# Kernel tuning notes

Hardware: AMD Instinct MI355X
Metric: run time of the kernel (lower is better)

## Reference

```python
import jax, jax.numpy as jnp
import numpy as np

B, T, C = 4, 2048, 1024   # batch, seq_len, n_embd
H, D = 16, 64             # num heads, head dim (H*D == C)


def setup_inputs() -> dict:
    key = jax.random.key(0)
    ks = jax.random.split(key, 6)
    scale = 0.02
    x = jax.random.normal(ks[0], (B, T, C), dtype=jnp.float32)
    Wq = jax.random.normal(ks[1], (H, C, D), dtype=jnp.float32) * scale
    Wk = jax.random.normal(ks[2], (H, C, D), dtype=jnp.float32) * scale
    Wv = jax.random.normal(ks[3], (H, C, D), dtype=jnp.float32) * scale
    Wp = jax.random.normal(ks[4], (C, C), dtype=jnp.float32) * scale
    bp = jnp.zeros((C,), dtype=jnp.float32)
    return {"x": x, "Wq": Wq, "Wk": Wk, "Wv": Wv, "Wp": Wp, "bp": bp}


def reference(x, Wq, Wk, Wv, Wp, bp):
    # Batched per-head projections (equivalent to the per-head nn.Linear loop)
    q = jnp.einsum('btc,hcd->bhtd', x, Wq)
    k = jnp.einsum('btc,hcd->bhtd', x, Wk)
    v = jnp.einsum('btc,hcd->bhtd', x, Wv)
    # NOTE: original code scales by C**-0.5 where C = n_embd (not head dim)
    scores = jnp.einsum('bhtd,bhsd->bhts', q, k) * (C ** -0.5)
    causal = jnp.tril(jnp.ones((T, T), dtype=bool))  # [T, T]
    scores = jnp.where(causal, scores, -jnp.inf)
    att = jax.nn.softmax(scores, axis=-1)            # [B, H, T, T]
    out = jnp.einsum('bhts,bhsd->bhtd', att, v)      # [B, H, T, D]
    # concat heads (order matches torch.cat over head list) then output proj
    out = out.transpose(0, 2, 1, 3).reshape(B, T, H * D)
    return out @ Wp + bp
```

## Files before the change

### kernel.cpp

```cpp
#include <hip/hip_runtime.h>
#include <hip/hip_bf16.h>


#define B_ 4
#define T_ 2048
#define C_ 1024
#define H_ 16
#define D_ 64
#define M_ (B_*T_)

typedef unsigned short u16;
typedef unsigned short ushort8 __attribute__((ext_vector_type(8)));
typedef unsigned int uint4v __attribute__((ext_vector_type(4)));
typedef int int2v __attribute__((ext_vector_type(2)));
typedef __attribute__((ext_vector_type(8))) short bf16x8;
typedef __attribute__((ext_vector_type(16))) float f32x16;

__device__ __forceinline__ u16 f2bf(float f) {
    __hip_bfloat16 h = __float2bfloat16(f);
    return *reinterpret_cast<u16*>(&h);
}
__device__ __forceinline__ unsigned pkt(float lo, float hi2) {
    return __builtin_amdgcn_perm(__float_as_uint(hi2), __float_as_uint(lo), 0x07060302u);
}
__device__ __forceinline__ void gload_lds16(const void* g, void* lds) {
    __builtin_amdgcn_global_load_lds((const __attribute__((address_space(1))) unsigned int*)g,
                                     (__attribute__((address_space(3))) unsigned int*)lds, 16, 0, 0);
}
__device__ __forceinline__ int swz4(int r) { return (r ^ (r >> 2)) & 3; }

__global__ __launch_bounds__(256) void cast_x(const float* __restrict__ in, u16* __restrict__ out) {
    int i = (blockIdx.x * 256 + threadIdx.x) * 8;
    float4 a = *reinterpret_cast<const float4*>(in + i);
    float4 b = *reinterpret_cast<const float4*>(in + i + 4);
    ushort8 o;
    o[0]=f2bf(a.x); o[1]=f2bf(a.y); o[2]=f2bf(a.z); o[3]=f2bf(a.w);
    o[4]=f2bf(b.x); o[5]=f2bf(b.y); o[6]=f2bf(b.z); o[7]=f2bf(b.w);
    *reinterpret_cast<ushort8*>(out + i) = o;
}

__device__ __forceinline__ void ttile64(const float* __restrict__ in, int ldin,
                                        u16* __restrict__ out, int ldout, float scale) {
    __shared__ float t[64][65];
    const int tid = threadIdx.x;
    {
        int c = tid & 63, rr = tid >> 6;
        #pragma unroll
        for (int i = 0; i < 16; ++i) {
            int r = i * 4 + rr;
            t[r][c] = in[(size_t)r * ldin + c];
        }
    }
    __syncthreads();
    {
        int r2 = tid & 63, cg = tid >> 6;
        #pragma unroll
        for (int i = 0; i < 16; ++i) {
            int cc = i * 4 + cg;
            out[(size_t)cc * ldout + r2] = f2bf(t[r2][cc] * scale);
        }
    }
}

__global__ __launch_bounds__(256) void tw_qkv(const float* __restrict__ Wq, const float* __restrict__ Wk,
                                              const float* __restrict__ Wv, u16* __restrict__ Wt) {
    const int z = blockIdx.y;
    const int which = z >> 4, h = z & 15;
    const float* W = (which == 0 ? Wq : which == 1 ? Wk : Wv) + (size_t)h * C_ * D_;
    const int r0 = blockIdx.x * 64;
    const float scale = (which == 0) ? 0.03125f * 1.4426950408889634f : 1.f;
    ttile64(W + (size_t)r0 * D_, D_, Wt + (size_t)(which * 16 + h) * 64 * C_ + r0, C_, scale);
}

__global__ __launch_bounds__(256) void tw_p(const float* __restrict__ Wp, u16* __restrict__ Wpt) {
    const int r0 = blockIdx.x * 64, c0 = blockIdx.y * 64;
    ttile64(Wp + (size_t)r0 * C_ + c0, C_, Wpt + (size_t)c0 * C_ + r0, C_, 1.f);
}

__global__ __launch_bounds__(256) void tv(const u16* __restrict__ v, u16* __restrict__ vT) {
    __shared__ u16 t[64][72];
    const int tid = threadIdx.x;
    const int t0 = blockIdx.x * 64, bh = blockIdx.y;
    const u16* src = v + ((size_t)bh * T_ + t0) * D_;
    #pragma unroll
    for (int it = 0; it < 2; ++it) {
        int idx = it * 256 + tid;
        int r = idx >> 3, c8 = (idx & 7) * 8;
        *reinterpret_cast<ushort8*>(&t[r][c8]) =
            *reinterpret_cast<const ushort8*>(src + (size_t)r * D_ + c8);
    }
    __syncthreads();
    #pragma unroll
    for (int it = 0; it < 2; ++it) {
        int idx = it * 256 + tid;
        int d = idx >> 3, c8 = (idx & 7) * 8;
        ushort8 w;
        #pragma unroll
        for (int i = 0; i < 8; ++i) w[i] = t[c8 + i][d];
        *reinterpret_cast<ushort8*>(vT + ((size_t)bh * D_ + d) * T_ + t0 + c8) = w;
    }
}

__device__ __forceinline__ void gemm_core3(const u16* __restrict__ A, const u16* __restrict__ Bt,
                                           int m0, int n0, u16* lds, f32x16 (&acc)[4][2]) {
    const int tid = threadIdx.x;
    const int wid = tid >> 6, lane = tid & 63;
    const int l31 = lane & 31, hi = lane >> 5;
    const int wr = wid >> 1, wc = wid & 1;

    const u16* src[6];
    #pragma unroll
    for (int it = 0; it < 6; ++it) {
        int slot = it * 256 + tid;
        int row, g;
        const u16* base;
        if (it < 4) { row = slot >> 2; g = slot & 3; base = A + (size_t)(m0 + row) * C_; }
        else        { int s2 = slot - 1024; row = s2 >> 2; g = s2 & 3; base = Bt + (size_t)(n0 + row) * C_; }
        src[it] = base + ((g ^ swz4(row)) * 8);
    }

    const char* lb = reinterpret_cast<const char*>(lds);
    int aoff[2][4], boff[2][2];
    #pragma unroll
    for (int kk = 0; kk < 2; ++kk) {
        #pragma unroll
        for (int mt = 0; mt < 4; ++mt) {
            int row = wr * 128 + mt * 32 + l31;
            aoff[kk][mt] = row * 64 + (((kk * 2 + hi) ^ swz4(row)) & 3) * 16;
        }
        #pragma unroll
        for (int nt = 0; nt < 2; ++nt) {
            int row = wc * 64 + nt * 32 + l31;
            boff[kk][nt] = 16384 + row * 64 + (((kk * 2 + hi) ^ swz4(row)) & 3) * 16;
        }
    }

#define STG(BU16)                                                                   \
    {                                                                               \
        _Pragma("unroll")                                                           \
        for (int it = 0; it < 6; ++it) {                                            \
            gload_lds16(src[it], lds + (BU16) + (it * 256 + tid) * 8);              \
            src[it] += 32;                                                          \
        }                                                                           \
    }

    STG(0);
    STG(12288);

    #pragma unroll
    for (int t = 0; t < 32; ++t) {
        if (t < 31) { asm volatile("s_waitcnt vmcnt(6)" ::: "memory"); }
        else        { asm volatile("s_waitcnt vmcnt(0)" ::: "memory"); }
        __builtin_amdgcn_sched_barrier(0);
        __builtin_amdgcn_s_barrier();
        __builtin_amdgcn_sched_barrier(0);

        const char* lbuf = lb + (t & 1) * 24576;
        __builtin_amdgcn_s_setprio(1);
        #pragma unroll
        for (int kk = 0; kk < 2; ++kk) {
            bf16x8 bf0 = *reinterpret_cast<const bf16x8*>(lbuf + boff[kk][0]);
            bf16x8 bf1 = *reinterpret_cast<const bf16x8*>(lbuf + boff[kk][1]);
            #pragma unroll
            for (int mt = 0; mt < 4; ++mt) {
                bf16x8 af = *reinterpret_cast<const bf16x8*>(lbuf + aoff[kk][mt]);
                acc[mt][0] = __builtin_amdgcn_mfma_f32_32x32x16_bf16(af, bf0, acc[mt][0], 0, 0, 0);
                acc[mt][1] = __builtin_amdgcn_mfma_f32_32x32x16_bf16(af, bf1, acc[mt][1], 0, 0, 0);
            }
        }
        __builtin_amdgcn_s_setprio(0);
        __builtin_amdgcn_sched_barrier(0);
        __builtin_amdgcn_s_barrier();
        __builtin_amdgcn_sched_barrier(0);
        if (t + 2 < 32) STG((t & 1) * 12288);
    }
#undef STG
}

__global__ __launch_bounds__(256, 2) void qkv_gemm(const u16* __restrict__ xb, const u16* __restrict__ Wt,
                                                   u16* __restrict__ q, u16* __restrict__ k,
                                                   u16* __restrict__ v) {
    __shared__ u16 lds[2 * 12288];
    f32x16 acc[4][2];
    #pragma unroll
    for (int i = 0; i < 4; ++i)
        #pragma unroll
        for (int j = 0; j < 2; ++j)
            #pragma unroll
            for (int r = 0; r < 16; ++r) acc[i][j][r] = 0.f;
    const int m0 = blockIdx.x * 256, n0 = blockIdx.y * 128;
    gemm_core3(xb, Wt, m0, n0, lds, acc);

    const int tid = threadIdx.x, wid = tid >> 6, lane = tid & 63;
    const int l31 = lane & 31, hi = lane >> 5;
    const int wr = wid >> 1, wc = wid & 1;
    #pragma unroll
    for (int mt = 0; mt < 4; ++mt) {
        #pragma unroll
        for (int nt = 0; nt < 2; ++nt) {
            int n = n0 + wc * 64 + nt * 32 + l31;
            int which = n >> 10, h = (n >> 6) & 15, d = n & 63;
            u16* dst = (which == 0 ? q : which == 1 ? k : v);
            #pragma unroll
            for (int r = 0; r < 16; ++r) {
                int m = m0 + wr * 128 + mt * 32 + (r & 3) + 8 * (r >> 2) + 4 * hi;
                int b = m >> 11, t = m & (T_ - 1);
                dst[((size_t)(b * H_ + h) * T_ + t) * D_ + d] = f2bf(acc[mt][nt][r]);
            }
        }
    }
}

__global__ __launch_bounds__(256, 2) void out_gemm(const u16* __restrict__ ob, const u16* __restrict__ Wpt,
                                                   const float* __restrict__ bp, float* __restrict__ out) {
    __shared__ u16 lds[2 * 12288];
    f32x16 acc[4][2];
    #pragma unroll
    for (int i = 0; i < 4; ++i)
        #pragma unroll
        for (int j = 0; j < 2; ++j)
            #pragma unroll
            for (int r = 0; r < 16; ++r) acc[i][j][r] = 0.f;
    const int m0 = blockIdx.x * 256, n0 = blockIdx.y * 128;
    gemm_core3(ob, Wpt, m0, n0, lds, acc);

    const int tid = threadIdx.x, wid = tid >> 6, lane = tid & 63;
    const int l31 = lane & 31, hi = lane >> 5;
    const int wr = wid >> 1, wc = wid & 1;
    #pragma unroll
    for (int mt = 0; mt < 4; ++mt) {
        #pragma unroll
        for (int nt = 0; nt < 2; ++nt) {
            int n = n0 + wc * 64 + nt * 32 + l31;
            float bv = bp[n];
            #pragma unroll
            for (int r = 0; r < 16; ++r) {
                int m = m0 + wr * 128 + mt * 32 + (r & 3) + 8 * (r >> 2) + 4 * hi;
                out[(size_t)m * C_ + n] = acc[mt][nt][r] + bv;
            }
        }
    }
}

template<int CUR>
__device__ __forceinline__ void attn_tile(const char* const (&pf)[4], const bf16x8 (&qf)[4],
                                          const f32x16& z16, float& lrun,
                                          f32x16& oacc0, f32x16& oacc1,
                                          bool isdiag, int relq, int hi) {
    f32x16 st0, st1;
    __builtin_amdgcn_s_setprio(1);
    {
        bf16x8 ka0 = *reinterpret_cast<const bf16x8*>(pf[0] + CUR * 32768);
        bf16x8 ka1 = *reinterpret_cast<const bf16x8*>(pf[0] + CUR * 32768 + 4096);
        st0 = __builtin_amdgcn_mfma_f32_32x32x16_bf16(ka0, qf[0], z16, 0, 0, 0);
        st1 = __builtin_amdgcn_mfma_f32_32x32x16_bf16(ka1, qf[0], z16, 0, 0, 0);
    }
    #pragma unroll
    for (int kc = 1; kc < 4; ++kc) {
        bf16x8 ka0 = *reinterpret_cast<const bf16x8*>(pf[kc] + CUR * 32768);
        bf16x8 ka1 = *reinterpret_cast<const bf16x8*>(pf[kc] + CUR * 32768 + 4096);
        st0 = __builtin_amdgcn_mfma_f32_32x32x16_bf16(ka0, qf[kc], st0, 0, 0, 0);
        st1 = __builtin_amdgcn_mfma_f32_32x32x16_bf16(ka1, qf[kc], st1, 0, 0, 0);
    }
    __builtin_amdgcn_s_setprio(0);

    if (isdiag) {
        #pragma unroll
        for (int rr = 0; rr < 16; ++rr) {
            int sl = (rr & 3) + 8 * (rr >> 2) + 4 * hi;
            if (sl > relq)      st0[rr] = -INFINITY;
            if (sl + 32 > relq) st1[rr] = -INFINITY;
        }
    }

    float rsum = 0.f;
    #pragma unroll
    for (int rr = 0; rr < 16; ++rr) {
        st0[rr] = __builtin_amdgcn_exp2f(st0[rr]);
        st1[rr] = __builtin_amdgcn_exp2f(st1[rr]);
        rsum += st0[rr] + st1[rr];
    }
    rsum += __shfl_xor(rsum, 32);
    lrun += rsum;

    bf16x8 pa0, pa1, pa2, pa3;
#if __has_builtin(__builtin_amdgcn_permlane32_swap)
#define MK_PA(PA, SV, RB)                                                          \
    {                                                                              \
        int X0 = (int)pkt(SV[RB + 0], SV[RB + 1]);                                 \
        int X1 = (int)pkt(SV[RB + 2], SV[RB + 3]);                                 \
        int Y0 = (int)pkt(SV[RB + 4], SV[RB + 5]);                                 \
        int Y1 = (int)pkt(SV[RB + 6], SV[RB + 7]);                                 \
        int2v r0 = __builtin_amdgcn_permlane32_swap(X0, Y0, false, false);         \
        int2v r1 = __builtin_amdgcn_permlane32_swap(X1, Y1, false, false);         \
        uint4v w; w[0] = (unsigned)r0[0]; w[1] = (unsigned)r1[0];                  \
        w[2] = (unsigned)r0[1]; w[3] = (unsigned)r1[1];                            \
        PA = __builtin_bit_cast(bf16x8, w);                                        \
    }
#else
#define MK_PA(PA, SV, RB)                                                          \
    {                                                                              \
        unsigned X0 = pkt(SV[RB + 0], SV[RB + 1]);                                 \
        unsigned X1 = pkt(SV[RB + 2], SV[RB + 3]);                                 \
        unsigned Y0 = pkt(SV[RB + 4], SV[RB + 5]);                                 \
        unsigned sX0 = __shfl_xor(X0, 32), sY0 = __shfl_xor(Y0, 32);               \
        unsigned Y1 = pkt(SV[RB + 6], SV[RB + 7]);                                 \
        unsigned sX1 = __shfl_xor(X1, 32), sY1 = __shfl_xor(Y1, 32);               \
        uint4v w;                                                                  \
        w[0] = hi ? sY0 : X0; w[1] = hi ? sY1 : X1;                                \
        w[2] = hi ? Y0 : sX0; w[3] = hi ? Y1 : sX1;                                \
        PA = __builtin_bit_cast(bf16x8, w);                                        \
    }
#endif
    MK_PA(pa0, st0, 0); MK_PA(pa1, st0, 8); MK_PA(pa2, st1, 0); MK_PA(pa3, st1, 8);
#undef MK_PA

    __builtin_amdgcn_s_setprio(1);
#define PV_STEP(SCJ, PAV)                                                          \
    {                                                                              \
        bf16x8 va0 = *reinterpret_cast<const bf16x8*>(pf[SCJ] + CUR * 32768 + 16384);        \
        bf16x8 va1 = *reinterpret_cast<const bf16x8*>(pf[SCJ] + CUR * 32768 + 16384 + 4096); \
        oacc0 = __builtin_amdgcn_mfma_f32_32x32x16_bf16(va0, PAV, oacc0, 0, 0, 0); \
        oacc1 = __builtin_amdgcn_mfma_f32_32x32x16_bf16(va1, PAV, oacc1, 0, 0, 0); \
    }
    PV_STEP(0, pa0) PV_STEP(1, pa1) PV_STEP(2, pa2) PV_STEP(3, pa3)
#undef PV_STEP
    __builtin_amdgcn_s_setprio(0);
}

__global__ __launch_bounds__(512, 4) void attn_mfma(const u16* __restrict__ q,
                                                    const u16* __restrict__ k,
                                                    const u16* __restrict__ vT,
                                                    u16* __restrict__ o) {
    __shared__ u16 smem[32768];

    const int tid  = threadIdx.x;
    const int wid  = tid >> 6;
    const int lane = tid & 63;
    const int l31  = lane & 31;
    const int hi   = lane >> 5;

    const int lin = blockIdx.x;
    const int r   = lin & 255;
    const int f   = lin >> 8;
    const int bh  = r & 63;
    const int e   = r >> 6;
    const int qb  = f ? (7 - e) : e;

    const int q0 = qb * 256;
    const size_t base = (size_t)bh * T_ * D_;
    const u16* kp  = k  + base;
    const u16* vtp = vT + (size_t)bh * D_ * T_;
    const int qglob = q0 + wid * 32 + l31;

    bf16x8 qf[4];
    {
        const u16* qp = q + base + (size_t)qglob * D_;
        #pragma unroll
        for (int kc = 0; kc < 4; ++kc)
            qf[kc] = *reinterpret_cast<const bf16x8*>(qp + kc * 16 + hi * 8);
    }

    const int rw = tid >> 3;
    const int cg = (tid & 7) ^ (rw & 7);
    const u16* gK = kp  + (size_t)rw * D_ + cg * 8;
    const u16* gV = vtp + (size_t)rw * T_ + cg * 8;

    u16* sbase = &smem[0];
    u16* dK = sbase + tid * 8;
    u16* dV = sbase + 8192 + tid * 8;

    const char* pf[4];
    #pragma unroll
    for (int j = 0; j < 4; ++j)
        pf[j] = reinterpret_cast<const char*>(sbase) + l31 * 128 + (((j * 2 + hi) ^ (l31 & 7)) << 4);

    float lrun = 0.f;
    f32x16 oacc0, oacc1, z16;
    #pragma unroll
    for (int rr = 0; rr < 16; ++rr) { oacc0[rr] = 0.f; oacc1[rr] = 0.f; z16[rr] = 0.f; }

    const int ntile  = 4 * qb + 4;
    const int diag_t = 4 * qb + (wid >> 1);
    const int relq   = 32 * (wid & 1) + l31;

#define STG(BUFU16)                                                                \
    {                                                                              \
        gload_lds16(gK, dK + (BUFU16)); gload_lds16(gV, dV + (BUFU16));            \
        gK += 64 * D_; gV += 64;                                                   \
    }

    STG(0);
    __syncthreads();

    for (int tt = 0; tt < ntile; tt += 2) {
        if (tt + 1 < ntile) STG(16384);
        if (tt <= diag_t)
            attn_tile<0>(pf, qf, z16, lrun, oacc0, oacc1, tt == diag_t, relq, hi);
        __syncthreads();
        if (tt + 2 < ntile) STG(0);
        if (tt + 1 <= diag_t)
            attn_tile<1>(pf, qf, z16, lrun, oacc0, oacc1, tt + 1 == diag_t, relq, hi);
        __syncthreads();
    }
#undef STG

    float linv = 1.f / lrun;
    float* ot = reinterpret_cast<float*>(sbase) + wid * 2048;
    #pragma unroll
    for (int rr = 0; rr < 16; ++rr) {
        int d0v = (rr & 3) + 8 * (rr >> 2) + 4 * hi;
        int d1v = d0v + 32;
        ot[l31 * 64 + (((d0v >> 2) ^ (l31 & 7)) << 2) + (d0v & 3)] = oacc0[rr] * linv;
        ot[l31 * 64 + (((d1v >> 2) ^ (l31 & 7)) << 2) + (d1v & 3)] = oacc1[rr] * linv;
    }

    const int b = bh >> 4, h = bh & 15;
    const int qrow = lane >> 1;
    const int d0 = (lane & 1) * 32;
    u16 tmp[32];
    #pragma unroll
    for (int i = 0; i < 8; ++i) {
        int g = ((d0 >> 2) + i) ^ (qrow & 7);
        float4 fv = *reinterpret_cast<const float4*>(&ot[qrow * 64 + (g << 2)]);
        tmp[i * 4 + 0] = f2bf(fv.x); tmp[i * 4 + 1] = f2bf(fv.y);
        tmp[i * 4 + 2] = f2bf(fv.z); tmp[i * 4 + 3] = f2bf(fv.w);
    }
    u16* orow = o + ((size_t)b * T_ + q0 + wid * 32 + qrow) * C_ + h * 64 + d0;
    #pragma unroll
    for (int j = 0; j < 4; ++j)
        *reinterpret_cast<ushort8*>(orow + j * 8) = *reinterpret_cast<ushort8*>(&tmp[j * 8]);
}

extern "C" void kernel_launch(void* const* d_in, const int* in_sizes, int n_in,
                              void* d_out, int out_size, void* d_ws, size_t ws_size,
                              hipStream_t stream) {
    const float* x  = (const float*)d_in[0];
    const float* Wq = (const float*)d_in[1];
    const float* Wk = (const float*)d_in[2];
    const float* Wv = (const float*)d_in[3];
    const float* Wp = (const float*)d_in[4];
    const float* bp = (const float*)d_in[5];
    float* out = (float*)d_out;

    const size_t E = (size_t)M_ * C_;
    u16* xb  = (u16*)d_ws;
    u16* qb  = xb  + E;
    u16* kb  = qb  + E;
    u16* vb  = kb  + E;
    u16* obf = vb  + E;
    u16* Wt  = obf + E;
    u16* Wpt = Wt  + (size_t)3072 * 1024;
    u16* vTb = xb;

    cast_x<<<(E / 2048), 256, 0, stream>>>(x, xb);
    tw_qkv<<<dim3(16, 48), 256, 0, stream>>>(Wq, Wk, Wv, Wt);
    tw_p<<<dim3(16, 16), 256, 0, stream>>>(Wp, Wpt);

    qkv_gemm<<<dim3(M_ / 256, 3072 / 128), 256, 0, stream>>>(xb, Wt, qb, kb, vb);

    tv<<<dim3(T_ / 64, B_ * H_), 256, 0, stream>>>(vb, vTb);

    attn_mfma<<<dim3(512), 512, 0, stream>>>(qb, kb, vTb, obf);

    out_gemm<<<dim3(M_ / 256, C_ / 128), 256, 0, stream>>>(obf, Wpt, bp, out);
}
```

Measured before the change: 152.1 us.

## Rewrite QKV GEMM with 256x256 tiles, 512 threads and 16x16x32 MFMA

Replaces the QKV projection kernel with a dedicated 256x256-tile kernel using 8 waves, 16x16x32 bf16 MFMAs and a double-buffered 128 KB LDS with XOR-swizzled global-to-LDS loads over K=64 chunks. The larger output tile raises arithmetic intensity and reuse of A and B per LDS load, and the sub-tiled quad schedule interleaves LDS fragment loads with MFMA work. The cost is higher LDS and register pressure, and the output scatter becomes 16-bit strided stores.

```diff
diff --git a/kernel.cpp b/kernel.cpp
--- a/kernel.cpp
+++ b/kernel.cpp
@@ -14,6 +14,7 @@
 typedef unsigned int uint4v __attribute__((ext_vector_type(4)));
 typedef int int2v __attribute__((ext_vector_type(2)));
 typedef __attribute__((ext_vector_type(8))) short bf16x8;
+typedef __attribute__((ext_vector_type(4))) float f32x4;
 typedef __attribute__((ext_vector_type(16))) float f32x16;
 
 __device__ __forceinline__ u16 f2bf(float f) {
@@ -98,6 +99,123 @@
         #pragma unroll
         for (int i = 0; i < 8; ++i) w[i] = t[c8 + i][d];
         *reinterpret_cast<ushort8*>(vT + ((size_t)bh * D_ + d) * T_ + t0 + c8) = w;
+    }
+}
+
+__global__ __launch_bounds__(512, 2) void qkv_gemm(const u16* __restrict__ A, const u16* __restrict__ Bt,
+                                                   u16* __restrict__ q, u16* __restrict__ k,
+                                                   u16* __restrict__ v) {
+    __shared__ u16 lds[65536];
+    const int tid = threadIdx.x;
+    const int wid = tid >> 6, lane = tid & 63;
+    const int l16 = lane & 15, lq = lane >> 4;
+    const int wr = wid >> 2, wc = wid & 3;
+    const int m0 = blockIdx.x * 256, n0 = blockIdx.y * 256;
+
+    f32x4 acc[8][4];
+    #pragma unroll
+    for (int i = 0; i < 8; ++i)
+        #pragma unroll
+        for (int j = 0; j < 4; ++j) { acc[i][j][0]=0.f; acc[i][j][1]=0.f; acc[i][j][2]=0.f; acc[i][j][3]=0.f; }
+
+    const u16* gsrc[8];
+    int dstoff[8];
+    #pragma unroll
+    for (int u = 0; u < 8; ++u) {
+        int it = u & 1, h = (u >> 1) & 1;
+        int s = it * 512 + tid;
+        int row = s >> 3, g = s & 7;
+        int gs = (g ^ (row & 7)) * 8;
+        if (u < 4) gsrc[u] = A  + (size_t)(m0 + h * 128 + row) * C_ + gs;
+        else       gsrc[u] = Bt + (size_t)(n0 + h * 128 + row) * C_ + gs;
+        dstoff[u] = (u < 4 ? 0 : 32768) + h * 8192 + s * 8;
+    }
+
+    const char* lb = reinterpret_cast<const char*>(lds);
+    const int gA0 = (lq ^ (l16 & 7)) * 16;
+    const int gA1 = ((4 + lq) ^ (l16 & 7)) * 16;
+    const char* pA0 = lb + wr * 16384 + l16 * 128 + gA0;
+    const char* pA1 = lb + wr * 16384 + l16 * 128 + gA1;
+    const char* pB0 = lb + 65536 + (wc >> 1) * 16384 + ((wc & 1) * 64 + l16) * 128 + gA0;
+    const char* pB1 = lb + 65536 + (wc >> 1) * 16384 + ((wc & 1) * 64 + l16) * 128 + gA1;
+
+#define STAGE8(DSTD)                                                                 \
+    {                                                                                \
+        _Pragma("unroll")                                                            \
+        for (int u = 0; u < 8; ++u) {                                                \
+            gload_lds16(gsrc[u], lds + (DSTD) + dstoff[u]);                          \
+            gsrc[u] += 64;                                                           \
+        }                                                                            \
+    }
+
+#define QUAD(D, MB, NB)                                                              \
+    {                                                                                \
+        __builtin_amdgcn_s_setprio(1);                                               \
+        _Pragma("unroll")                                                            \
+        for (int kk = 0; kk < 2; ++kk)                                               \
+            _Pragma("unroll")                                                        \
+            for (int mt = 0; mt < 4; ++mt)                                           \
+                _Pragma("unroll")                                                    \
+                for (int nt = 0; nt < 2; ++nt)                                       \
+                    acc[(MB) + mt][(NB) + nt] = __builtin_amdgcn_mfma_f32_16x16x32_bf16( \
+                        Af[mt][kk], Bf[nt][kk], acc[(MB) + mt][(NB) + nt], 0, 0, 0); \
+        __builtin_amdgcn_s_setprio(0);                                               \
+        __builtin_amdgcn_sched_barrier(0);                                           \
+    }
+
+#define LDA(D, MB)                                                                   \
+    _Pragma("unroll")                                                                \
+    for (int mt = 0; mt < 4; ++mt) {                                                 \
+        Af[mt][0] = *reinterpret_cast<const bf16x8*>(pA0 + (D) * 32768 + ((MB) + mt) * 2048); \
+        Af[mt][1] = *reinterpret_cast<const bf16x8*>(pA1 + (D) * 32768 + ((MB) + mt) * 2048); \
+    }
+
+#define LDB(D, NB)                                                                   \
+    _Pragma("unroll")                                                                \
+    for (int nt = 0; nt < 2; ++nt) {                                                 \
+        Bf[nt][0] = *reinterpret_cast<const bf16x8*>(pB0 + (D) * 32768 + ((NB) + nt) * 2048); \
+        Bf[nt][1] = *reinterpret_cast<const bf16x8*>(pB1 + (D) * 32768 + ((NB) + nt) * 2048); \
+    }
+
+#define QTILE(D, SEN)                                                                \
+    {                                                                                \
+        asm volatile("s_waitcnt vmcnt(0)" ::: "memory");                             \
+        __builtin_amdgcn_sched_barrier(0);                                           \
+        __builtin_amdgcn_s_barrier();                                                \
+        __builtin_amdgcn_sched_barrier(0);                                           \
+        if (SEN) STAGE8(((D) ^ 1) * 16384);                                          \
+        bf16x8 Af[4][2], Bf[2][2];                                                   \
+        LDA(D, 0); LDB(D, 0); QUAD(D, 0, 0);          \
+        LDB(D, 2); QUAD(D, 0, 2);                    \
+        LDA(D, 4); QUAD(D, 4, 2);                    \
+        LDB(D, 0); QUAD(D, 4, 0);                     \
+    }
+
+    STAGE8(0);
+    for (int tt = 0; tt < 8; ++tt) {
+        QTILE(0, true);
+        QTILE(1, tt != 7);
+    }
+#undef QTILE
+#undef LDA
+#undef LDB
+#undef QUAD
+#undef STAGE8
+
+    #pragma unroll
+    for (int mt = 0; mt < 8; ++mt) {
+        #pragma unroll
+        for (int j = 0; j < 4; ++j) {
+            int m = m0 + wr * 128 + mt * 16 + lq * 4 + j;
+            int b = m >> 11, t = m & (T_ - 1);
+            #pragma unroll
+            for (int nt = 0; nt < 4; ++nt) {
+                int n = n0 + wc * 64 + nt * 16 + l16;
+                int which = n >> 10, h = (n >> 6) & 15, d = n & 63;
+                u16* dst = (which == 0 ? q : which == 1 ? k : v);
+                dst[((size_t)(b * H_ + h) * T_ + t) * D_ + d] = f2bf(acc[mt][nt][j]);
+            }
+        }
     }
 }
 
@@ -175,40 +293,6 @@
         if (t + 2 < 32) STG((t & 1) * 12288);
     }
 #undef STG
-}
-
-__global__ __launch_bounds__(256, 2) void qkv_gemm(const u16* __restrict__ xb, const u16* __restrict__ Wt,
-                                                   u16* __restrict__ q, u16* __restrict__ k,
-                                                   u16* __restrict__ v) {
-    __shared__ u16 lds[2 * 12288];
-    f32x16 acc[4][2];
-    #pragma unroll
-    for (int i = 0; i < 4; ++i)
-        #pragma unroll
-        for (int j = 0; j < 2; ++j)
-            #pragma unroll
-            for (int r = 0; r < 16; ++r) acc[i][j][r] = 0.f;
-    const int m0 = blockIdx.x * 256, n0 = blockIdx.y * 128;
-    gemm_core3(xb, Wt, m0, n0, lds, acc);
-
-    const int tid = threadIdx.x, wid = tid >> 6, lane = tid & 63;
-    const int l31 = lane & 31, hi = lane >> 5;
-    const int wr = wid >> 1, wc = wid & 1;
-    #pragma unroll
-    for (int mt = 0; mt < 4; ++mt) {
-        #pragma unroll
-        for (int nt = 0; nt < 2; ++nt) {
-            int n = n0 + wc * 64 + nt * 32 + l31;
-            int which = n >> 10, h = (n >> 6) & 15, d = n & 63;
-            u16* dst = (which == 0 ? q : which == 1 ? k : v);
-            #pragma unroll
-            for (int r = 0; r < 16; ++r) {
-                int m = m0 + wr * 128 + mt * 32 + (r & 3) + 8 * (r >> 2) + 4 * hi;
-                int b = m >> 11, t = m & (T_ - 1);
-                dst[((size_t)(b * H_ + h) * T_ + t) * D_ + d] = f2bf(acc[mt][nt][r]);
-            }
-        }
-    }
 }
 
 __global__ __launch_bounds__(256, 2) void out_gemm(const u16* __restrict__ ob, const u16* __restrict__ Wpt,
@@ -457,7 +541,7 @@
     tw_qkv<<<dim3(16, 48), 256, 0, stream>>>(Wq, Wk, Wv, Wt);
     tw_p<<<dim3(16, 16), 256, 0, stream>>>(Wp, Wpt);
 
-    qkv_gemm<<<dim3(M_ / 256, 3072 / 128), 256, 0, stream>>>(xb, Wt, qb, kb, vb);
+    qkv_gemm<<<dim3(M_ / 256, 3072 / 256), 512, 0, stream>>>(xb, Wt, qb, kb, vb);
 
     tv<<<dim3(T_ / 64, B_ * H_), 256, 0, stream>>>(vb, vTb);
 
```

New measurement: 153.3 us. Within noise of the previous version (+0.8%).

## Merge prep kernels and write V transposed directly from QKV GEMM epilogue

Applied to the files above, without the earlier changes.

Folds the x cast and both weight-transpose kernels into one prep launch that dispatches on block index. The QKV GEMM epilogue now writes V straight into the transposed [b,h,d,t] layout with packed 4-element stores, which removes the separate V transpose kernel and its extra read and write of V. This saves three kernel launches and one full pass over V. The cost is a strided, partly scattered store pattern for V in the GEMM epilogue.

```diff
diff --git a/kernel.cpp b/kernel.cpp
--- a/kernel.cpp
+++ b/kernel.cpp
@@ -10,6 +10,7 @@
 #define M_ (B_*T_)
 
 typedef unsigned short u16;
+typedef unsigned short ushort4v __attribute__((ext_vector_type(4)));
 typedef unsigned short ushort8 __attribute__((ext_vector_type(8)));
 typedef unsigned int uint4v __attribute__((ext_vector_type(4)));
 typedef int int2v __attribute__((ext_vector_type(2)));
@@ -28,16 +29,6 @@
                                      (__attribute__((address_space(3))) unsigned int*)lds, 16, 0, 0);
 }
 __device__ __forceinline__ int swz4(int r) { return (r ^ (r >> 2)) & 3; }
-
-__global__ __launch_bounds__(256) void cast_x(const float* __restrict__ in, u16* __restrict__ out) {
-    int i = (blockIdx.x * 256 + threadIdx.x) * 8;
-    float4 a = *reinterpret_cast<const float4*>(in + i);
-    float4 b = *reinterpret_cast<const float4*>(in + i + 4);
-    ushort8 o;
-    o[0]=f2bf(a.x); o[1]=f2bf(a.y); o[2]=f2bf(a.z); o[3]=f2bf(a.w);
-    o[4]=f2bf(b.x); o[5]=f2bf(b.y); o[6]=f2bf(b.z); o[7]=f2bf(b.w);
-    *reinterpret_cast<ushort8*>(out + i) = o;
-}
 
 __device__ __forceinline__ void ttile64(const float* __restrict__ in, int ldin,
                                         u16* __restrict__ out, int ldout, float scale) {
@@ -62,42 +53,31 @@
     }
 }
 
-__global__ __launch_bounds__(256) void tw_qkv(const float* __restrict__ Wq, const float* __restrict__ Wk,
-                                              const float* __restrict__ Wv, u16* __restrict__ Wt) {
-    const int z = blockIdx.y;
-    const int which = z >> 4, h = z & 15;
-    const float* W = (which == 0 ? Wq : which == 1 ? Wk : Wv) + (size_t)h * C_ * D_;
-    const int r0 = blockIdx.x * 64;
-    const float scale = (which == 0) ? 0.03125f * 1.4426950408889634f : 1.f;
-    ttile64(W + (size_t)r0 * D_, D_, Wt + (size_t)(which * 16 + h) * 64 * C_ + r0, C_, scale);
-}
-
-__global__ __launch_bounds__(256) void tw_p(const float* __restrict__ Wp, u16* __restrict__ Wpt) {
-    const int r0 = blockIdx.x * 64, c0 = blockIdx.y * 64;
-    ttile64(Wp + (size_t)r0 * C_ + c0, C_, Wpt + (size_t)c0 * C_ + r0, C_, 1.f);
-}
-
-__global__ __launch_bounds__(256) void tv(const u16* __restrict__ v, u16* __restrict__ vT) {
-    __shared__ u16 t[64][72];
-    const int tid = threadIdx.x;
-    const int t0 = blockIdx.x * 64, bh = blockIdx.y;
-    const u16* src = v + ((size_t)bh * T_ + t0) * D_;
-    #pragma unroll
-    for (int it = 0; it < 2; ++it) {
-        int idx = it * 256 + tid;
-        int r = idx >> 3, c8 = (idx & 7) * 8;
-        *reinterpret_cast<ushort8*>(&t[r][c8]) =
-            *reinterpret_cast<const ushort8*>(src + (size_t)r * D_ + c8);
-    }
-    __syncthreads();
-    #pragma unroll
-    for (int it = 0; it < 2; ++it) {
-        int idx = it * 256 + tid;
-        int d = idx >> 3, c8 = (idx & 7) * 8;
-        ushort8 w;
-        #pragma unroll
-        for (int i = 0; i < 8; ++i) w[i] = t[c8 + i][d];
-        *reinterpret_cast<ushort8*>(vT + ((size_t)bh * D_ + d) * T_ + t0 + c8) = w;
+__global__ __launch_bounds__(256) void prep(const float* __restrict__ x,
+                                            const float* __restrict__ Wq, const float* __restrict__ Wk,
+                                            const float* __restrict__ Wv, const float* __restrict__ Wp,
+                                            u16* __restrict__ xb, u16* __restrict__ Wt,
+                                            u16* __restrict__ Wpt) {
+    const int bid = blockIdx.x;
+    if (bid < 4096) {
+        int i = (bid * 256 + threadIdx.x) * 8;
+        float4 a = *reinterpret_cast<const float4*>(x + i);
+        float4 b = *reinterpret_cast<const float4*>(x + i + 4);
+        ushort8 o;
+        o[0]=f2bf(a.x); o[1]=f2bf(a.y); o[2]=f2bf(a.z); o[3]=f2bf(a.w);
+        o[4]=f2bf(b.x); o[5]=f2bf(b.y); o[6]=f2bf(b.z); o[7]=f2bf(b.w);
+        *reinterpret_cast<ushort8*>(xb + i) = o;
+    } else if (bid < 4096 + 768) {
+        int idx = bid - 4096;
+        int r0 = (idx & 15) * 64, z = idx >> 4;
+        int which = z >> 4, h = z & 15;
+        const float* W = (which == 0 ? Wq : which == 1 ? Wk : Wv) + (size_t)h * C_ * D_;
+        const float scale = (which == 0) ? 0.03125f * 1.4426950408889634f : 1.f;
+        ttile64(W + (size_t)r0 * D_, D_, Wt + (size_t)(which * 16 + h) * 64 * C_ + r0, C_, scale);
+    } else {
+        int idx = bid - 4864;
+        int r0 = (idx & 15) * 64, c0 = (idx >> 4) * 64;
+        ttile64(Wp + (size_t)r0 * C_ + c0, C_, Wpt + (size_t)c0 * C_ + r0, C_, 1.f);
     }
 }
 
@@ -179,7 +159,7 @@
 
 __global__ __launch_bounds__(256, 2) void qkv_gemm(const u16* __restrict__ xb, const u16* __restrict__ Wt,
                                                    u16* __restrict__ q, u16* __restrict__ k,
-                                                   u16* __restrict__ v) {
+                                                   u16* __restrict__ vT) {
     __shared__ u16 lds[2 * 12288];
     f32x16 acc[4][2];
     #pragma unroll
@@ -200,12 +180,27 @@
         for (int nt = 0; nt < 2; ++nt) {
             int n = n0 + wc * 64 + nt * 32 + l31;
             int which = n >> 10, h = (n >> 6) & 15, d = n & 63;
-            u16* dst = (which == 0 ? q : which == 1 ? k : v);
-            #pragma unroll
-            for (int r = 0; r < 16; ++r) {
-                int m = m0 + wr * 128 + mt * 32 + (r & 3) + 8 * (r >> 2) + 4 * hi;
-                int b = m >> 11, t = m & (T_ - 1);
-                dst[((size_t)(b * H_ + h) * T_ + t) * D_ + d] = f2bf(acc[mt][nt][r]);
+            if (which < 2) {
+                u16* dst = (which == 0 ? q : k);
+                #pragma unroll
+                for (int r = 0; r < 16; ++r) {
+                    int m = m0 + wr * 128 + mt * 32 + (r & 3) + 8 * (r >> 2) + 4 * hi;
+                    int b = m >> 11, t = m & (T_ - 1);
+                    dst[((size_t)(b * H_ + h) * T_ + t) * D_ + d] = f2bf(acc[mt][nt][r]);
+                }
+            } else {
+                #pragma unroll
+                for (int rq = 0; rq < 4; ++rq) {
+                    int m = m0 + wr * 128 + mt * 32 + 8 * rq + 4 * hi;
+                    int b = m >> 11, t = m & (T_ - 1);
+                    ushort4v pk;
+                    pk[0] = f2bf(acc[mt][nt][rq * 4 + 0]);
+                    pk[1] = f2bf(acc[mt][nt][rq * 4 + 1]);
+                    pk[2] = f2bf(acc[mt][nt][rq * 4 + 2]);
+                    pk[3] = f2bf(acc[mt][nt][rq * 4 + 3]);
+                    *reinterpret_cast<ushort4v*>(
+                        vT + ((size_t)(b * H_ + h) * D_ + d) * T_ + t) = pk;
+                }
             }
         }
     }
@@ -447,19 +442,14 @@
     u16* xb  = (u16*)d_ws;
     u16* qb  = xb  + E;
     u16* kb  = qb  + E;
-    u16* vb  = kb  + E;
-    u16* obf = vb  + E;
+    u16* vTb = kb  + E;
+    u16* obf = vTb + E;
     u16* Wt  = obf + E;
     u16* Wpt = Wt  + (size_t)3072 * 1024;
-    u16* vTb = xb;
-
-    cast_x<<<(E / 2048), 256, 0, stream>>>(x, xb);
-    tw_qkv<<<dim3(16, 48), 256, 0, stream>>>(Wq, Wk, Wv, Wt);
-    tw_p<<<dim3(16, 16), 256, 0, stream>>>(Wp, Wpt);
-
-    qkv_gemm<<<dim3(M_ / 256, 3072 / 128), 256, 0, stream>>>(xb, Wt, qb, kb, vb);
-
-    tv<<<dim3(T_ / 64, B_ * H_), 256, 0, stream>>>(vb, vTb);
+
+    prep<<<dim3(5120), 256, 0, stream>>>(x, Wq, Wk, Wv, Wp, xb, Wt, Wpt);
+
+    qkv_gemm<<<dim3(M_ / 256, 3072 / 128), 256, 0, stream>>>(xb, Wt, qb, kb, vTb);
 
     attn_mfma<<<dim3(512), 512, 0, stream>>>(qb, kb, vTb, obf);
 
```

Result: faster. 142.1 us (-6.6%).
